# Kernel optimization log

Hardware: AMD Instinct MI355X
Metric: run time of the kernel (lower is better)

Reference implementation:

```python
import math
import jax, jax.numpy as jnp
import numpy as np

R, N, B, E, H, M = 128, 256, 1, 512, 8, 4
D = E // H
NEG = -1e9  # eye-mask fill value from masked_fill(-1000000000)


def setup_inputs() -> dict:
    key = jax.random.key(0)
    ks = jax.random.split(key, 10)
    p = lambda k, shape: jax.random.normal(k, shape, jnp.float32) * 0.02
    z = lambda n: jnp.zeros((n,), jnp.float32)
    return {
        "x": jax.random.normal(ks[0], (R, N, B, E), jnp.float32),
        "network": jax.random.uniform(ks[1], (B, N, N, M), jnp.float32),
        "Wq": p(ks[2], (E, E)), "bq": z(E),
        "Wk": p(ks[3], (E, E)), "bk": z(E),
        "Wv": p(ks[4], (E, E)), "bv": z(E),
        "Wo": p(ks[5], (E, E)), "bo": z(E),
        "Wq1": p(ks[6], (D, 8)), "bq1": z(8),
        "Wk1": p(ks[7], (1, 8)), "bk1": z(8),
        "l": jax.random.normal(ks[8], (H, 1, 1, 1), jnp.float32),
    }


def reference(x, network, Wq, bq, Wk, bk, Wv, bv, Wo, bo, Wq1, bq1, Wk1, bk1, l):
    # x: [R, N, B, E]; network: [B, N, N, M] (B must be 1, as in the torch module)
    scaling = (D ** -0.5) / math.sqrt(R)  # align_scaling

    q = (x @ Wq + bq).reshape(R, N, B, H, D) * scaling
    k = (x @ Wk + bk).reshape(R, N, B, H, D)

    # shared contraction: summed over rows r, kept per head-dim d -> [H, B, N, N, D]
    qk = jnp.einsum('rinhd,rjnhd->hnijd', q, k)

    # network-bias MLP branch
    q1 = (qk @ Wq1 + bq1).mean(0)                  # [B, N, N, 8]
    network_k = network[..., None] * Wk1[0] + bk1  # Linear(1,8): [B, N, N, M, 8]
    net_attn = jnp.einsum('nijd,nijmd->nijm', q1, network_k)  # [B, N, N, M]
    net_attn = jnp.tile(net_attn, (H, 1, 1, 1))    # repeat over heads (B==1) -> [H, N, N, M]

    # attn_weights 'rinhd,rjnhd->hnij' == qk summed over d
    attn_weights = qk.sum(-1)                      # [H, B, N, N]

    net_probs = jax.nn.softmax(net_attn, axis=-1)  # softmax over M network channels
    net_bias = (network * net_probs).sum(-1)[:, None, :, :]  # [H, 1(B), N, N]
    attn_weights = attn_weights + l * net_bias

    eye = jnp.eye(N, dtype=bool)
    attn_weights = jnp.where(eye, NEG, attn_weights)
    attn_probs = jax.nn.softmax(attn_weights, axis=-1)  # [H, B, N, N]

    v = (x @ Wv + bv).reshape(R, N, B, H, D)
    context = jnp.einsum('hnij,rjnhd->rinhd', attn_probs, v).reshape(R, N, B, E)
    output = context @ Wo + bo
    return (output, attn_probs, l)
```

## Files before the change

kernel.cpp:

```cpp
#include <hip/hip_runtime.h>
#include <hip/hip_bf16.h>
#include <cmath>
#include <stdint.h>

using bf16 = __hip_bfloat16;
typedef __attribute__((ext_vector_type(8))) short bf16x8;
typedef __attribute__((ext_vector_type(4))) float f32x4;

constexpr long HS = 2097152;

__device__ __forceinline__ void gload16(const bf16* g, bf16* l)
{
  __builtin_amdgcn_global_load_lds(
      (const __attribute__((address_space(1))) void*)g,
      (__attribute__((address_space(3))) void*)l,
      16, 0, 0);
}

__device__ __forceinline__ int swsrc(int c) { return (((c & 3) ^ ((c >> 3) & 3)) * 8); }

__global__ __launch_bounds__(256)
void k_convert_x(const float* __restrict__ x, bf16* __restrict__ xb)
{
  const long idx = (long)blockIdx.x * 256 + threadIdx.x;
  const float4 f0 = *(const float4*)&x[idx * 8];
  const float4 f1 = *(const float4*)&x[idx * 8 + 4];
  alignas(16) bf16 t[8] = {
    __float2bfloat16(f0.x), __float2bfloat16(f0.y),
    __float2bfloat16(f0.z), __float2bfloat16(f0.w),
    __float2bfloat16(f1.x), __float2bfloat16(f1.y),
    __float2bfloat16(f1.z), __float2bfloat16(f1.w)};
  *(uint4*)&xb[idx * 8] = *(const uint4*)t;
}

__global__ __launch_bounds__(256)
void k_prep_w(const float* __restrict__ Wq, const float* __restrict__ Wk,
              const float* __restrict__ Wv, const float* __restrict__ Wo,
              bf16* __restrict__ WT, float scaling)
{
  const int sel = blockIdx.z;
  const float* W = sel == 0 ? Wq : sel == 1 ? Wk : sel == 2 ? Wv : Wo;
  const float sc = sel == 0 ? scaling : 1.0f;
  const int k0 = blockIdx.x * 64, n0 = blockIdx.y * 64;
  __shared__ float tile[64][68];
  const int tid = threadIdx.x;
  #pragma unroll
  for (int it = 0; it < 4; it++) {
    const int c = tid + it * 256;
    const int kk = c >> 4, nn4 = (c & 15) * 4;
    const float4 v = *(const float4*)&W[(long)(k0 + kk) * 512 + n0 + nn4];
    tile[kk][nn4] = v.x; tile[kk][nn4 + 1] = v.y;
    tile[kk][nn4 + 2] = v.z; tile[kk][nn4 + 3] = v.w;
  }
  __syncthreads();
  #pragma unroll
  for (int it = 0; it < 2; it++) {
    const int c = tid + it * 256;
    const int nn = c >> 3, k8 = (c & 7) * 8;
    alignas(16) bf16 t[8];
    #pragma unroll
    for (int jj = 0; jj < 8; jj++) t[jj] = __float2bfloat16(tile[k8 + jj][nn] * sc);
    *(uint4*)&WT[(long)(sel * 512 + n0 + nn) * 512 + k0 + k8] = *(const uint4*)t;
  }
}

__global__ void k_prep_small(const float* __restrict__ bq, const float* __restrict__ bk,
                             const float* __restrict__ bv, const float* __restrict__ bo,
                             const float* __restrict__ Wq1, const float* __restrict__ Wk1,
                             float* __restrict__ bias_all, float* __restrict__ u, float scaling)
{
  const int idx = blockIdx.x * 256 + threadIdx.x;
  const int s2 = idx >> 9, n2 = idx & 511;
  const float* b = s2 == 0 ? bq : s2 == 1 ? bk : s2 == 2 ? bv : bo;
  bias_all[idx] = b[n2] * (s2 == 0 ? scaling : 1.0f);
  if (idx < 64) {
    float s = 0.0f;
    #pragma unroll
    for (int c = 0; c < 8; c++) s += Wq1[idx * 8 + c] * Wk1[c];
    u[idx] = s;
  }
}

__global__ __launch_bounds__(256)
void gemm_qkv(const bf16* __restrict__ xb, const bf16* __restrict__ WT,
              const float* __restrict__ bias_all,
              bf16* __restrict__ Qn, bf16* __restrict__ Kn, bf16* __restrict__ Vj)
{
  __shared__ __align__(16) unsigned short smem[24576];
  bf16* As = (bf16*)smem;
  bf16* Bs = (bf16*)smem + 12288;
  const int tid = threadIdx.x, lane = tid & 63;
  const int wid = tid >> 6, wr = wid >> 1, wc = wid & 1;
  const int lr = lane & 15;
  const int lkx = ((lane >> 4) ^ ((lane >> 1) & 3)) * 8;
  const int flat = (blockIdx.x & 7) * 384 + (blockIdx.x >> 3);
  const int m0 = (flat / 12) * 128, n0 = (flat % 12) * 128;
  const int c1 = tid + 256;
  const int ra0 = tid >> 2, ra1 = c1 >> 2;
  const int ps = swsrc(tid);
  f32x4 acc[4][4] = {};

  auto stage = [&](int b, int k0) {
    gload16(&xb[(long)(m0 + ra0) * 512 + k0 + ps], &As[b * 4096 + tid * 8]);
    gload16(&xb[(long)(m0 + ra1) * 512 + k0 + ps], &As[b * 4096 + c1 * 8]);
    gload16(&WT[(long)(n0 + ra0) * 512 + k0 + ps], &Bs[b * 4096 + tid * 8]);
    gload16(&WT[(long)(n0 + ra1) * 512 + k0 + ps], &Bs[b * 4096 + c1 * 8]);
  };

  stage(0, 0);
  stage(1, 32);

  for (int t = 0; t < 16; ++t) {
    const int cur = t % 3;
    if (t < 14) {
      stage((t + 2) % 3, (t + 2) * 32);
      asm volatile("s_waitcnt vmcnt(8)" ::: "memory");
    } else if (t == 14) {
      asm volatile("s_waitcnt vmcnt(4)" ::: "memory");
    } else {
      asm volatile("s_waitcnt vmcnt(0)" ::: "memory");
    }
    __builtin_amdgcn_s_barrier();
    bf16x8 af[4], bfr[4];
    #pragma unroll
    for (int m = 0; m < 4; m++)
      af[m] = *(const bf16x8*)&As[cur * 4096 + (wr * 64 + m * 16 + lr) * 32 + lkx];
    #pragma unroll
    for (int n = 0; n < 4; n++)
      bfr[n] = *(const bf16x8*)&Bs[cur * 4096 + (wc * 64 + n * 16 + lr) * 32 + lkx];
    #pragma unroll
    for (int m = 0; m < 4; m++)
      #pragma unroll
      for (int n = 0; n < 4; n++)
        acc[m][n] = __builtin_amdgcn_mfma_f32_16x16x32_bf16(af[m], bfr[n], acc[m][n], 0, 0, 0);
    __builtin_amdgcn_s_barrier();
  }

  const int er = (lane >> 4) * 4, ec = lane & 15;
  if (n0 < 1024) {
    #pragma unroll
    for (int m = 0; m < 4; m++) {
      const int row0 = m0 + wr * 64 + m * 16 + er;
      #pragma unroll
      for (int n = 0; n < 4; n++) {
        const int col = n0 + wc * 64 + n * 16 + ec;
        const float bv = bias_all[col];
        #pragma unroll
        for (int q = 0; q < 4; q++) {
          const float v = acc[m][n][q] + bv;
          const long row = row0 + q;
          if (col < 512) Qn[row * 512 + col]       = __float2bfloat16(v);
          else           Kn[row * 512 + col - 512] = __float2bfloat16(v);
        }
      }
    }
  } else {
    bf16* vt = (bf16*)smem;
    #pragma unroll
    for (int m = 0; m < 4; m++) {
      const int rt0 = wr * 64 + m * 16 + er;
      #pragma unroll
      for (int n = 0; n < 4; n++) {
        const int ct = wc * 64 + n * 16 + ec;
        const float bv = bias_all[n0 + ct];
        #pragma unroll
        for (int q = 0; q < 4; q++)
          vt[(rt0 + q) * 140 + ct] = __float2bfloat16(acc[m][n][q] + bv);
      }
    }
    __syncthreads();
    const int r = m0 >> 8, tok0 = m0 & 255;
    #pragma unroll
    for (int cc = 0; cc < 8; cc++) {
      const int c = cc * 256 + tid;
      const int ct2 = c & 127, i8 = (c >> 7) * 8;
      alignas(16) bf16 tmp[8];
      #pragma unroll
      for (int t = 0; t < 8; t++) tmp[t] = vt[(i8 + t) * 140 + ct2];
      const int hd = n0 - 1024 + ct2;
      const int h = hd >> 6, d = hd & 63;
      *(uint4*)&Vj[(long)h * HS + (long)(r * 64 + d) * 256 + tok0 + i8] = *(const uint4*)tmp;
    }
  }
}

__global__ __launch_bounds__(256)
void gemm_logits(const bf16* __restrict__ Qn, const bf16* __restrict__ Kn,
                 const float* __restrict__ u, float* __restrict__ part)
{
  __shared__ bf16 As[3][128 * 32];
  __shared__ bf16 Bs[3][128 * 32];
  __shared__ float us[64];
  const int tid = threadIdx.x, lane = tid & 63;
  const int wid = tid >> 6, wr = wid >> 1, wc = wid & 1;
  const int lr = lane & 15;
  const int lkx = ((lane >> 4) ^ ((lane >> 1) & 3)) * 8;
  const int z = blockIdx.z, batch = z >> 3, ks = z & 7, h = batch & 7;
  const bool uscale = batch >= 8;
  const int m0 = blockIdx.y * 128, n0 = blockIdx.x * 128;
  if (tid < 64) us[tid] = u[tid];
  __syncthreads();
  const int c1 = tid + 256;
  const int ra0 = tid >> 2, ra1 = c1 >> 2;
  const int ps = swsrc(tid);
  f32x4 acc[4][4] = {};

  auto gk_of = [&](int kk) { return ks * 1024 + kk * 32; };

  if (!uscale) {
    auto stage = [&](int b, int kk) {
      const int gk = gk_of(kk), r = gk >> 6, d0 = gk & 63;
      const long ab = (long)(r * 256 + m0) * 512 + h * 64 + d0;
      const long bb = (long)(r * 256 + n0) * 512 + h * 64 + d0;
      gload16(&Qn[ab + (long)ra0 * 512 + ps], &As[b][tid * 8]);
      gload16(&Qn[ab + (long)ra1 * 512 + ps], &As[b][c1 * 8]);
      gload16(&Kn[bb + (long)ra0 * 512 + ps], &Bs[b][tid * 8]);
      gload16(&Kn[bb + (long)ra1 * 512 + ps], &Bs[b][c1 * 8]);
    };
    stage(0, 0);
    stage(1, 1);
    for (int kk = 0; kk < 32; ++kk) {
      const int cur = kk % 3;
      if (kk < 30) {
        stage((kk + 2) % 3, kk + 2);
        asm volatile("s_waitcnt vmcnt(8)" ::: "memory");
      } else if (kk == 30) {
        asm volatile("s_waitcnt vmcnt(4)" ::: "memory");
      } else {
        asm volatile("s_waitcnt vmcnt(0)" ::: "memory");
      }
      __builtin_amdgcn_s_barrier();
      bf16x8 af[4], bfr[4];
      #pragma unroll
      for (int m = 0; m < 4; m++)
        af[m] = *(const bf16x8*)&As[cur][(wr * 64 + m * 16 + lr) * 32 + lkx];
      #pragma unroll
      for (int n = 0; n < 4; n++)
        bfr[n] = *(const bf16x8*)&Bs[cur][(wc * 64 + n * 16 + lr) * 32 + lkx];
      #pragma unroll
      for (int m = 0; m < 4; m++)
        #pragma unroll
        for (int n = 0; n < 4; n++)
          acc[m][n] = __builtin_amdgcn_mfma_f32_16x16x32_bf16(af[m], bfr[n], acc[m][n], 0, 0, 0);
      __builtin_amdgcn_s_barrier();
    }
  } else {
    {
      const int gk = gk_of(0), r = gk >> 6, d0 = gk & 63;
      const long ab = (long)(r * 256 + m0) * 512 + h * 64 + d0;
      const long bb = (long)(r * 256 + n0) * 512 + h * 64 + d0;
      gload16(&Kn[bb + (long)ra0 * 512 + ps], &Bs[0][tid * 8]);
      gload16(&Kn[bb + (long)ra1 * 512 + ps], &Bs[0][c1 * 8]);
      const uint4 v0 = *(const uint4*)&Qn[ab + (long)ra0 * 512 + ps];
      const uint4 v1 = *(const uint4*)&Qn[ab + (long)ra1 * 512 + ps];
      const unsigned short* p0 = (const unsigned short*)&v0;
      const unsigned short* p1 = (const unsigned short*)&v1;
      alignas(16) bf16 t0[8], t1[8];
      #pragma unroll
      for (int jj = 0; jj < 8; jj++) {
        t0[jj] = __float2bfloat16(__bfloat162float(*(const bf16*)&p0[jj]) * us[d0 + ps + jj]);
        t1[jj] = __float2bfloat16(__bfloat162float(*(const bf16*)&p1[jj]) * us[d0 + ps + jj]);
      }
      *(uint4*)&As[0][tid * 8] = *(const uint4*)t0;
      *(uint4*)&As[0][c1 * 8] = *(const uint4*)t1;
    }
    __syncthreads();
    int buf = 0;
    for (int kk = 0; kk < 32; ++kk) {
      uint4 va0, va1;
      int d0n = 0;
      if (kk < 31) {
        const int gk = gk_of(kk + 1), r = gk >> 6;
        d0n = gk & 63;
        const long ab = (long)(r * 256 + m0) * 512 + h * 64 + d0n;
        const long bb = (long)(r * 256 + n0) * 512 + h * 64 + d0n;
        gload16(&Kn[bb + (long)ra0 * 512 + ps], &Bs[buf ^ 1][tid * 8]);
        gload16(&Kn[bb + (long)ra1 * 512 + ps], &Bs[buf ^ 1][c1 * 8]);
        va0 = *(const uint4*)&Qn[ab + (long)ra0 * 512 + ps];
        va1 = *(const uint4*)&Qn[ab + (long)ra1 * 512 + ps];
      }
      bf16x8 af[4], bfr[4];
      #pragma unroll
      for (int m = 0; m < 4; m++)
        af[m] = *(const bf16x8*)&As[buf][(wr * 64 + m * 16 + lr) * 32 + lkx];
      #pragma unroll
      for (int n = 0; n < 4; n++)
        bfr[n] = *(const bf16x8*)&Bs[buf][(wc * 64 + n * 16 + lr) * 32 + lkx];
      #pragma unroll
      for (int m = 0; m < 4; m++)
        #pragma unroll
        for (int n = 0; n < 4; n++)
          acc[m][n] = __builtin_amdgcn_mfma_f32_16x16x32_bf16(af[m], bfr[n], acc[m][n], 0, 0, 0);
      if (kk < 31) {
        const unsigned short* p0 = (const unsigned short*)&va0;
        const unsigned short* p1 = (const unsigned short*)&va1;
        alignas(16) bf16 t0[8], t1[8];
        #pragma unroll
        for (int jj = 0; jj < 8; jj++) {
          t0[jj] = __float2bfloat16(__bfloat162float(*(const bf16*)&p0[jj]) * us[d0n + ps + jj]);
          t1[jj] = __float2bfloat16(__bfloat162float(*(const bf16*)&p1[jj]) * us[d0n + ps + jj]);
        }
        *(uint4*)&As[buf ^ 1][tid * 8] = *(const uint4*)t0;
        *(uint4*)&As[buf ^ 1][c1 * 8] = *(const uint4*)t1;
      }
      __syncthreads();
      buf ^= 1;
    }
  }

  float* C = part + (long)z * 65536;
  const int er = (lane >> 4) * 4, ec = lane & 15;
  #pragma unroll
  for (int m = 0; m < 4; m++)
    #pragma unroll
    for (int n = 0; n < 4; n++) {
      const int col = n0 + wc * 64 + n * 16 + ec;
      #pragma unroll
      for (int q = 0; q < 4; q++)
        C[(long)(m0 + wr * 64 + m * 16 + er + q) * 256 + col] = acc[m][n][q];
    }
}

__global__ __launch_bounds__(256)
void gemm_ctx(const bf16* __restrict__ Pb, const bf16* __restrict__ Vj,
              bf16* __restrict__ ctxb)
{
  __shared__ bf16 As[3][128 * 32];
  __shared__ bf16 Bs[3][128 * 32];
  const int tid = threadIdx.x, lane = tid & 63;
  const int wid = tid >> 6, wr = wid >> 1, wc = wid & 1;
  const int lr = lane & 15;
  const int lkx = ((lane >> 4) ^ ((lane >> 1) & 3)) * 8;
  const int m0 = blockIdx.y * 128, n0 = blockIdx.x * 128, h = blockIdx.z;
  const bf16* A = Pb + (long)h * 65536;
  const bf16* B = Vj + (long)h * HS;
  const int c1 = tid + 256;
  const int ra0 = tid >> 2, ra1 = c1 >> 2;
  const int ps = swsrc(tid);
  f32x4 acc[4][4] = {};

  auto stage = [&](int b, int k0) {
    gload16(&A[(long)(m0 + ra0) * 256 + k0 + ps], &As[b][tid * 8]);
    gload16(&A[(long)(m0 + ra1) * 256 + k0 + ps], &As[b][c1 * 8]);
    gload16(&B[(long)(n0 + ra0) * 256 + k0 + ps], &Bs[b][tid * 8]);
    gload16(&B[(long)(n0 + ra1) * 256 + k0 + ps], &Bs[b][c1 * 8]);
  };

  stage(0, 0);
  stage(1, 32);

  for (int t = 0; t < 8; ++t) {
    const int cur = t % 3;
    if (t < 6) {
      stage((t + 2) % 3, (t + 2) * 32);
      asm volatile("s_waitcnt vmcnt(8)" ::: "memory");
    } else if (t == 6) {
      asm volatile("s_waitcnt vmcnt(4)" ::: "memory");
    } else {
      asm volatile("s_waitcnt vmcnt(0)" ::: "memory");
    }
    __builtin_amdgcn_s_barrier();
    bf16x8 af[4], bfr[4];
    #pragma unroll
    for (int m = 0; m < 4; m++)
      af[m] = *(const bf16x8*)&As[cur][(wr * 64 + m * 16 + lr) * 32 + lkx];
    #pragma unroll
    for (int n = 0; n < 4; n++)
      bfr[n] = *(const bf16x8*)&Bs[cur][(wc * 64 + n * 16 + lr) * 32 + lkx];
    #pragma unroll
    for (int m = 0; m < 4; m++)
      #pragma unroll
      for (int n = 0; n < 4; n++)
        acc[m][n] = __builtin_amdgcn_mfma_f32_16x16x32_bf16(af[m], bfr[n], acc[m][n], 0, 0, 0);
    __builtin_amdgcn_s_barrier();
  }

  const int er = (lane >> 4) * 4, ec = lane & 15;
  #pragma unroll
  for (int m = 0; m < 4; m++) {
    const int i0 = m0 + wr * 64 + m * 16 + er;
    #pragma unroll
    for (int n = 0; n < 4; n++) {
      const int col = n0 + wc * 64 + n * 16 + ec;
      const int rr = col >> 6, dd = col & 63;
      #pragma unroll
      for (int q = 0; q < 4; q++)
        ctxb[(long)(rr * 256 + i0 + q) * 512 + h * 64 + dd] = __float2bfloat16(acc[m][n][q]);
    }
  }
}

__global__ __launch_bounds__(512)
void gemm_outp(const bf16* __restrict__ A, const bf16* __restrict__ B,
               float* __restrict__ C, const float* __restrict__ bias)
{
  __shared__ bf16 As[3][128 * 32];
  __shared__ bf16 Bs[3][256 * 32];
  const int tid = threadIdx.x, lane = tid & 63, wid = tid >> 6;
  const int wr = wid >> 2, wc = wid & 3;
  const int lr = lane & 15;
  const int lkx = ((lane >> 4) ^ ((lane >> 1) & 3)) * 8;
  const int m0 = blockIdx.y * 128, n0 = blockIdx.x * 256;
  const int ra = tid >> 2;
  const int cb1 = tid + 512;
  const int rb0 = tid >> 2, rb1 = cb1 >> 2;
  const int ps = swsrc(tid);
  f32x4 acc[4][4] = {};

  auto stage = [&](int b, int k0) {
    gload16(&A[(long)(m0 + ra) * 512 + k0 + ps], &As[b][tid * 8]);
    gload16(&B[(long)(n0 + rb0) * 512 + k0 + ps], &Bs[b][tid * 8]);
    gload16(&B[(long)(n0 + rb1) * 512 + k0 + ps], &Bs[b][cb1 * 8]);
  };

  stage(0, 0);
  stage(1, 32);

  for (int t = 0; t < 16; ++t) {
    const int cur = t % 3;
    if (t < 14) {
      stage((t + 2) % 3, (t + 2) * 32);
      asm volatile("s_waitcnt vmcnt(6)" ::: "memory");
    } else if (t == 14) {
      asm volatile("s_waitcnt vmcnt(3)" ::: "memory");
    } else {
      asm volatile("s_waitcnt vmcnt(0)" ::: "memory");
    }
    __builtin_amdgcn_s_barrier();
    bf16x8 af[4], bfr[4];
    #pragma unroll
    for (int m = 0; m < 4; m++)
      af[m] = *(const bf16x8*)&As[cur][(wr * 64 + m * 16 + lr) * 32 + lkx];
    #pragma unroll
    for (int n = 0; n < 4; n++)
      bfr[n] = *(const bf16x8*)&Bs[cur][(wc * 64 + n * 16 + lr) * 32 + lkx];
    #pragma unroll
    for (int m = 0; m < 4; m++)
      #pragma unroll
      for (int n = 0; n < 4; n++)
        acc[m][n] = __builtin_amdgcn_mfma_f32_16x16x32_bf16(af[m], bfr[n], acc[m][n], 0, 0, 0);
    __builtin_amdgcn_s_barrier();
  }

  const int er = (lane >> 4) * 4, ec = lane & 15;
  #pragma unroll
  for (int m = 0; m < 4; m++) {
    const int row0 = m0 + wr * 64 + m * 16 + er;
    #pragma unroll
    for (int n = 0; n < 4; n++) {
      const int col = n0 + wc * 64 + n * 16 + ec;
      const float bv = bias[col];
      #pragma unroll
      for (int q = 0; q < 4; q++)
        C[(long)(row0 + q) * 512 + col] = acc[m][n][q] + bv;
    }
  }
}

__global__ void k_bias(const float* __restrict__ part, const float* __restrict__ network,
                       const float* __restrict__ bq1, const float* __restrict__ Wk1,
                       float* __restrict__ net_bias)
{
  const int i = blockIdx.x, j = threadIdx.x;
  float c1 = 0.0f;
  #pragma unroll
  for (int c = 0; c < 8; c++) c1 += bq1[c] * Wk1[c];
  float s1 = 0.0f;
  const long ij = i * 256 + j;
  #pragma unroll
  for (int s = 64; s < 128; s++) s1 += part[(long)s * 65536 + ij];
  s1 = 0.125f * s1 + c1;
  const float4 nw = *(const float4*)&network[ij * 4];
  const float a0 = nw.x * s1, a1 = nw.y * s1, a2 = nw.z * s1, a3 = nw.w * s1;
  const float mx = fmaxf(fmaxf(a0, a1), fmaxf(a2, a3));
  const float e0 = expf(a0 - mx), e1 = expf(a1 - mx), e2 = expf(a2 - mx), e3 = expf(a3 - mx);
  const float inv = 1.0f / (e0 + e1 + e2 + e3);
  net_bias[ij] = (nw.x * e0 + nw.y * e1 + nw.z * e2 + nw.w * e3) * inv;
}

__global__ void k_softmax(const float* __restrict__ part, const float* __restrict__ net_bias,
                          const float* __restrict__ l, float* __restrict__ out_probs,
                          bf16* __restrict__ Pb, float* __restrict__ out_l)
{
  const int i = blockIdx.x, h = blockIdx.y, j = threadIdx.x;
  const long ij = i * 256 + j;
  float w = 0.0f;
  #pragma unroll
  for (int ks = 0; ks < 8; ks++) w += part[(long)(h * 8 + ks) * 65536 + ij];
  w += l[h] * net_bias[ij];
  if (j == i) w = -1e9f;
  float m = w;
  #pragma unroll
  for (int o = 32; o; o >>= 1) m = fmaxf(m, __shfl_xor(m, o));
  __shared__ float red[4], red2[4];
  if ((j & 63) == 0) red[j >> 6] = m;
  __syncthreads();
  m = fmaxf(fmaxf(red[0], red[1]), fmaxf(red[2], red[3]));
  const float e = expf(w - m);
  float s = e;
  #pragma unroll
  for (int o = 32; o; o >>= 1) s += __shfl_xor(s, o);
  if ((j & 63) == 0) red2[j >> 6] = s;
  __syncthreads();
  s = red2[0] + red2[1] + red2[2] + red2[3];
  const float p = e / s;
  out_probs[(long)h * 65536 + ij] = p;
  Pb[(long)h * 65536 + ij] = __float2bfloat16(p);
  if (h == 0 && i == 0 && j < 8) out_l[j] = l[j];
}

extern "C" void kernel_launch(void* const* d_in, const int* in_sizes, int n_in,
                              void* d_out, int out_size, void* d_ws, size_t ws_size,
                              hipStream_t stream)
{
  const float* x   = (const float*)d_in[0];
  const float* net = (const float*)d_in[1];
  const float* Wq  = (const float*)d_in[2];
  const float* bq  = (const float*)d_in[3];
  const float* Wk  = (const float*)d_in[4];
  const float* bk  = (const float*)d_in[5];
  const float* Wv  = (const float*)d_in[6];
  const float* bv  = (const float*)d_in[7];
  const float* Wo  = (const float*)d_in[8];
  const float* bo  = (const float*)d_in[9];
  const float* Wq1 = (const float*)d_in[10];
  const float* bq1 = (const float*)d_in[11];
  const float* Wk1 = (const float*)d_in[12];
  const float* l   = (const float*)d_in[14];
  float* out = (float*)d_out;

  bf16* Qn = (bf16*)d_out;
  bf16* Kn = Qn + 16777216;

  char* ws = (char*)d_ws;
  size_t off = 0;
  auto alloc = [&](size_t bytes) { char* p = ws + off; off += (bytes + 255) & ~255ULL; return p; };
  bf16*  WT       = (bf16*)alloc(2048ULL * 512 * 2);
  float* bias_all = (float*)alloc(2048 * 4);
  float* u        = (float*)alloc(64 * 4);
  bf16*  xb       = (bf16*)alloc(16777216ULL * 2);
  bf16*  Vj       = (bf16*)alloc(16777216ULL * 2);
  float* net_bias = (float*)alloc(65536ULL * 4);
  bf16*  Pb       = (bf16*)alloc(8ULL * 65536 * 2);
  float* part     = (float*)xb;
  bf16*  ctxb     = xb;

  const float scaling = (float)(0.125 / sqrt(128.0));

  k_convert_x<<<8192, 256, 0, stream>>>(x, xb);
  k_prep_w<<<dim3(8, 8, 4), 256, 0, stream>>>(Wq, Wk, Wv, Wo, WT, scaling);
  k_prep_small<<<8, 256, 0, stream>>>(bq, bk, bv, bo, Wq1, Wk1, bias_all, u, scaling);

  gemm_qkv<<<3072, 256, 0, stream>>>(xb, WT, bias_all, Qn, Kn, Vj);

  gemm_logits<<<dim3(2, 2, 128), 256, 0, stream>>>(Qn, Kn, u, part);

  k_bias<<<256, 256, 0, stream>>>(part, net, bq1, Wk1, net_bias);
  k_softmax<<<dim3(256, 8, 1), 256, 0, stream>>>(part, net_bias, l,
                                                 out + 16777216, Pb, out + 17301504);

  gemm_ctx<<<dim3(64, 2, 8), 256, 0, stream>>>(Pb, Vj, ctxb);

  gemm_outp<<<dim3(2, 256, 1), 512, 0, stream>>>(ctxb, WT + 1536 * 512, out, bias_all + 1536);
}
```

Measured before the change: 204.3 us.

## Enlarge QKV GEMM tile to 256x256 with 512 threads and one barrier per step

The QKV projection GEMM moves from 128x128 tiles with 256 threads to 256x256 tiles with 512 threads (8 waves, each computing 128x64). Larger tiles raise arithmetic intensity and cut redundant global/L2 traffic. The K loop now uses a single barrier per iteration, with the wait placed after the MFMAs so loads overlap compute. The V-transpose epilogue is rewritten to stage one 64-column slab at a time through shared memory, with wider coalesced stores. Doubled LDS and accumulator registers may reduce occupancy, and the grid shrinks from 3072 to 768 blocks.

```diff
diff --git a/kernel.cpp b/kernel.cpp
--- a/kernel.cpp
+++ b/kernel.cpp
@@ -81,30 +81,30 @@
   }
 }
 
-__global__ __launch_bounds__(256)
+__global__ __launch_bounds__(512, 2)
 void gemm_qkv(const bf16* __restrict__ xb, const bf16* __restrict__ WT,
               const float* __restrict__ bias_all,
               bf16* __restrict__ Qn, bf16* __restrict__ Kn, bf16* __restrict__ Vj)
 {
-  __shared__ __align__(16) unsigned short smem[24576];
+  __shared__ __align__(16) unsigned short smem[49152];
   bf16* As = (bf16*)smem;
-  bf16* Bs = (bf16*)smem + 12288;
+  bf16* Bs = (bf16*)smem + 24576;
   const int tid = threadIdx.x, lane = tid & 63;
-  const int wid = tid >> 6, wr = wid >> 1, wc = wid & 1;
+  const int wid = tid >> 6, wr = wid >> 2, wc = wid & 3;
   const int lr = lane & 15;
   const int lkx = ((lane >> 4) ^ ((lane >> 1) & 3)) * 8;
-  const int flat = (blockIdx.x & 7) * 384 + (blockIdx.x >> 3);
-  const int m0 = (flat / 12) * 128, n0 = (flat % 12) * 128;
-  const int c1 = tid + 256;
+  const int flat = ((int)blockIdx.x & 7) * 96 + ((int)blockIdx.x >> 3);
+  const int m0 = (flat / 6) * 256, nt = flat % 6, n0 = nt * 256;
+  const int c1 = tid + 512;
   const int ra0 = tid >> 2, ra1 = c1 >> 2;
-  const int ps = swsrc(tid);
-  f32x4 acc[4][4] = {};
+  const int ps0 = swsrc(tid), ps1 = swsrc(c1);
+  f32x4 acc[8][4] = {};
 
   auto stage = [&](int b, int k0) {
-    gload16(&xb[(long)(m0 + ra0) * 512 + k0 + ps], &As[b * 4096 + tid * 8]);
-    gload16(&xb[(long)(m0 + ra1) * 512 + k0 + ps], &As[b * 4096 + c1 * 8]);
-    gload16(&WT[(long)(n0 + ra0) * 512 + k0 + ps], &Bs[b * 4096 + tid * 8]);
-    gload16(&WT[(long)(n0 + ra1) * 512 + k0 + ps], &Bs[b * 4096 + c1 * 8]);
+    gload16(&xb[(long)(m0 + ra0) * 512 + k0 + ps0], &As[b * 8192 + tid * 8]);
+    gload16(&xb[(long)(m0 + ra1) * 512 + k0 + ps1], &As[b * 8192 + c1 * 8]);
+    gload16(&WT[(long)(n0 + ra0) * 512 + k0 + ps0], &Bs[b * 8192 + tid * 8]);
+    gload16(&WT[(long)(n0 + ra1) * 512 + k0 + ps1], &Bs[b * 8192 + c1 * 8]);
   };
 
   stage(0, 0);
@@ -112,74 +112,75 @@
 
   for (int t = 0; t < 16; ++t) {
     const int cur = t % 3;
-    if (t < 14) {
-      stage((t + 2) % 3, (t + 2) * 32);
+    if (t < 14) stage((t + 2) % 3, (t + 2) * 32);
+    if (t == 0) {
       asm volatile("s_waitcnt vmcnt(8)" ::: "memory");
-    } else if (t == 14) {
-      asm volatile("s_waitcnt vmcnt(4)" ::: "memory");
-    } else {
-      asm volatile("s_waitcnt vmcnt(0)" ::: "memory");
-    }
-    __builtin_amdgcn_s_barrier();
-    bf16x8 af[4], bfr[4];
-    #pragma unroll
-    for (int m = 0; m < 4; m++)
-      af[m] = *(const bf16x8*)&As[cur * 4096 + (wr * 64 + m * 16 + lr) * 32 + lkx];
+      __builtin_amdgcn_s_barrier();
+    }
+    bf16x8 af[8], bfr[4];
     #pragma unroll
     for (int n = 0; n < 4; n++)
-      bfr[n] = *(const bf16x8*)&Bs[cur * 4096 + (wc * 64 + n * 16 + lr) * 32 + lkx];
-    #pragma unroll
-    for (int m = 0; m < 4; m++)
+      bfr[n] = *(const bf16x8*)&Bs[cur * 8192 + (wc * 64 + n * 16 + lr) * 32 + lkx];
+    #pragma unroll
+    for (int m = 0; m < 8; m++)
+      af[m] = *(const bf16x8*)&As[cur * 8192 + (wr * 128 + m * 16 + lr) * 32 + lkx];
+    #pragma unroll
+    for (int m = 0; m < 8; m++)
       #pragma unroll
       for (int n = 0; n < 4; n++)
         acc[m][n] = __builtin_amdgcn_mfma_f32_16x16x32_bf16(af[m], bfr[n], acc[m][n], 0, 0, 0);
+    if (t < 14)       asm volatile("s_waitcnt vmcnt(4)" ::: "memory");
+    else if (t == 14) asm volatile("s_waitcnt vmcnt(0)" ::: "memory");
     __builtin_amdgcn_s_barrier();
   }
 
   const int er = (lane >> 4) * 4, ec = lane & 15;
-  if (n0 < 1024) {
-    #pragma unroll
-    for (int m = 0; m < 4; m++) {
-      const int row0 = m0 + wr * 64 + m * 16 + er;
+  if (nt < 4) {
+    bf16* dst = (nt < 2) ? Qn : Kn;
+    const int cb = (nt < 2) ? n0 : n0 - 512;
+    #pragma unroll
+    for (int m = 0; m < 8; m++) {
+      const int row0 = m0 + wr * 128 + m * 16 + er;
       #pragma unroll
       for (int n = 0; n < 4; n++) {
-        const int col = n0 + wc * 64 + n * 16 + ec;
-        const float bv = bias_all[col];
+        const int cw = wc * 64 + n * 16 + ec;
+        const float bv = bias_all[n0 + cw];
         #pragma unroll
-        for (int q = 0; q < 4; q++) {
-          const float v = acc[m][n][q] + bv;
-          const long row = row0 + q;
-          if (col < 512) Qn[row * 512 + col]       = __float2bfloat16(v);
-          else           Kn[row * 512 + col - 512] = __float2bfloat16(v);
-        }
+        for (int q = 0; q < 4; q++)
+          dst[(long)(row0 + q) * 512 + cb + cw] = __float2bfloat16(acc[m][n][q] + bv);
       }
     }
   } else {
     bf16* vt = (bf16*)smem;
-    #pragma unroll
-    for (int m = 0; m < 4; m++) {
-      const int rt0 = wr * 64 + m * 16 + er;
-      #pragma unroll
-      for (int n = 0; n < 4; n++) {
-        const int ct = wc * 64 + n * 16 + ec;
-        const float bv = bias_all[n0 + ct];
+    const int r = m0 >> 8;
+    const int hdbase = (nt - 4) * 256;
+    #pragma unroll 1
+    for (int p = 0; p < 4; ++p) {
+      __syncthreads();
+      if (wc == p) {
         #pragma unroll
-        for (int q = 0; q < 4; q++)
-          vt[(rt0 + q) * 140 + ct] = __float2bfloat16(acc[m][n][q] + bv);
-      }
-    }
-    __syncthreads();
-    const int r = m0 >> 8, tok0 = m0 & 255;
-    #pragma unroll
-    for (int cc = 0; cc < 8; cc++) {
-      const int c = cc * 256 + tid;
-      const int ct2 = c & 127, i8 = (c >> 7) * 8;
-      alignas(16) bf16 tmp[8];
-      #pragma unroll
-      for (int t = 0; t < 8; t++) tmp[t] = vt[(i8 + t) * 140 + ct2];
-      const int hd = n0 - 1024 + ct2;
-      const int h = hd >> 6, d = hd & 63;
-      *(uint4*)&Vj[(long)h * HS + (long)(r * 64 + d) * 256 + tok0 + i8] = *(const uint4*)tmp;
+        for (int m = 0; m < 8; m++) {
+          const int rt0 = wr * 128 + m * 16 + er;
+          #pragma unroll
+          for (int n = 0; n < 4; n++) {
+            const int ct = n * 16 + ec;
+            const float bv = bias_all[n0 + p * 64 + ct];
+            #pragma unroll
+            for (int q = 0; q < 4; q++)
+              vt[ct * 264 + rt0 + q] = __float2bfloat16(acc[m][n][q] + bv);
+          }
+        }
+      }
+      __syncthreads();
+      #pragma unroll
+      for (int cc = 0; cc < 4; cc++) {
+        const int c = cc * 512 + tid;
+        const int hl = c >> 5, tok8 = (c & 31) * 8;
+        const uint4 v = *(const uint4*)&vt[hl * 264 + tok8];
+        const int hd = hdbase + p * 64 + hl;
+        const int h = hd >> 6, d = hd & 63;
+        *(uint4*)&Vj[(long)h * HS + (long)(r * 64 + d) * 256 + tok8] = v;
+      }
     }
   }
 }
@@ -551,7 +552,7 @@
   k_prep_w<<<dim3(8, 8, 4), 256, 0, stream>>>(Wq, Wk, Wv, Wo, WT, scaling);
   k_prep_small<<<8, 256, 0, stream>>>(bq, bk, bv, bo, Wq1, Wk1, bias_all, u, scaling);
 
-  gemm_qkv<<<3072, 256, 0, stream>>>(xb, WT, bias_all, Qn, Kn, Vj);
+  gemm_qkv<<<768, 512, 0, stream>>>(xb, WT, bias_all, Qn, Kn, Vj);
 
   gemm_logits<<<dim3(2, 2, 128), 256, 0, stream>>>(Qn, Kn, u, part);
 
```

After: 200.4 us. About the same (-1.9%).
